# Kernel optimization log

Hardware: AMD Instinct MI355X
Metric: run time of the kernel (lower is better)

The kernel has to match this reference:

```python
import jax, jax.numpy as jnp
import numpy as np
from jax.ops import segment_sum

N0 = 50000
N1 = 50000
E = 300000
D = 128
L = 3
EPS_GIN = 0.1
COEF = 0.1
BN_EPS = 1e-5


def setup_inputs() -> dict:
    key = jax.random.key(0)
    ks = jax.random.split(key, 32)
    inp = {}
    inp['x0'] = jax.random.randint(ks[0], (N0, 2), 0, 3)
    inp['x1'] = jax.random.randint(ks[1], (N1, 2), 0, 3)
    inp['ei101'] = jax.random.randint(ks[2], (2, E), 0, N1)
    inp['ea101'] = jax.random.randint(ks[3], (E, 2), 0, 3)
    inp['ei110'] = jax.random.randint(ks[4], (2, E), 0, N0)  # src '1' -> dst '0' (N1==N0)
    inp['ea110'] = jax.random.randint(ks[5], (E, 2), 0, 3)
    inp['ei021'] = jax.random.randint(ks[6], (2, E), 0, N1)  # src '0' -> dst '1'
    inp['ea021'] = jax.random.randint(ks[7], (E, 2), 0, 3)
    inp['ei030'] = jax.random.randint(ks[8], (2, E), 0, N0)
    inp['ea030'] = jax.random.randint(ks[9], (E, 2), 0, 3)
    # learned parameters
    s = 0.05
    inp['x_emb1'] = jax.random.normal(ks[10], (120, D), jnp.float32) * s
    inp['x_emb2'] = jax.random.normal(ks[11], (3, D), jnp.float32) * s
    inp['e_emb1'] = jax.random.normal(ks[12], (6, D), jnp.float32) * s
    inp['e_emb2'] = jax.random.normal(ks[13], (3, D), jnp.float32) * s
    w = 1.0 / np.sqrt(D)
    inp['gin_w1'] = jax.random.normal(ks[14], (D, 2 * D), jnp.float32) * w
    inp['gin_b1'] = jnp.zeros((2 * D,), jnp.float32)
    inp['gin_w2'] = jax.random.normal(ks[15], (2 * D, D), jnp.float32) * (1.0 / np.sqrt(2 * D))
    inp['gin_b2'] = jnp.zeros((D,), jnp.float32)
    inp['w110'] = jax.random.normal(ks[16], (D, D), jnp.float32) * w
    inp['b110'] = jnp.zeros((D,), jnp.float32)
    inp['w021'] = jax.random.normal(ks[17], (D, D), jnp.float32) * w
    inp['b021'] = jnp.zeros((D,), jnp.float32)
    inp['w030'] = jax.random.normal(ks[18], (D, D), jnp.float32) * w
    inp['b030'] = jnp.zeros((D,), jnp.float32)
    inp['bn_gamma'] = jnp.ones((L, D), jnp.float32)
    inp['bn_beta'] = jnp.zeros((L, D), jnp.float32)
    return inp


def _add_self_loops(ei, ea, n):
    loop = jnp.arange(n, dtype=ei.dtype)
    ei = jnp.concatenate([ei, jnp.stack([loop, loop])], axis=1)
    self_attr = jnp.tile(jnp.array([[4, 0]], dtype=ea.dtype), (n, 1))
    return ei, jnp.concatenate([ea, self_attr], axis=0)


def _bn(x, gamma, beta):
    # training-mode BatchNorm1d: batch statistics, biased variance
    mu = jnp.mean(x, axis=0)
    var = jnp.var(x, axis=0)
    return (x - mu) * jax.lax.rsqrt(var + BN_EPS) * gamma + beta


def reference(x0, x1, ei101, ea101, ei110, ea110, ei021, ea021, ei030, ea030,
              x_emb1, x_emb2, e_emb1, e_emb2,
              gin_w1, gin_b1, gin_w2, gin_b2,
              w110, b110, w021, b021, w030, b030,
              bn_gamma, bn_beta):
    n0, n1 = x0.shape[0], x1.shape[0]
    # AddSelfLoops only for homogeneous edge types, fill_value=[4,0]
    ei101, ea101 = _add_self_loops(ei101, ea101, n1)
    ei030, ea030 = _add_self_loops(ei030, ea030, n0)

    h0 = x_emb1[x0[:, 0]] + x_emb2[x0[:, 1]]
    h1 = x_emb1[x1[:, 0]] + x_emb2[x1[:, 1]]
    e101 = e_emb1[ea101[:, 0]] + e_emb2[ea101[:, 1]]
    e110 = e_emb1[ea110[:, 0]] + e_emb2[ea110[:, 1]]
    e021 = e_emb1[ea021[:, 0]] + e_emb2[ea021[:, 1]]
    e030 = e_emb1[ea030[:, 0]] + e_emb2[ea030[:, 1]]

    def gin(h_src, h_dst, ei, eattr):
        agg = segment_sum(h_src[ei[0]] + eattr, ei[1], num_segments=h_dst.shape[0])
        z = agg + (1.0 + EPS_GIN) * h_dst
        return jnp.maximum(z @ gin_w1 + gin_b1, 0.0) @ gin_w2 + gin_b2

    def lin(h_src, n_dst, ei, eattr, w, b):
        agg = segment_sum(h_src[ei[0]] + eattr, ei[1], num_segments=n_dst)
        return (agg @ w + b) * COEF

    for layer in range(L):
        # HeteroConv aggr='mean' over convs sharing a destination node type
        out1 = 0.5 * (gin(h1, h1, ei101, e101) + lin(h0, n1, ei021, e021, w021, b021))
        out0 = 0.5 * (lin(h1, n0, ei110, e110, w110, b110) + lin(h0, n0, ei030, e030, w030, b030))
        g, b = bn_gamma[layer], bn_beta[layer]
        h0, h1 = _bn(out0, g, b), _bn(out1, g, b)
        if layer < L - 1:
            h0, h1 = jax.nn.relu(h0), jax.nn.relu(h1)
    # to_homogeneous().x: node types in order '0', '1'
    return jnp.concatenate([h0, h1], axis=0)
```

## Files before the change

### kernel.cpp

```cpp
#include <hip/hip_runtime.h>

#define D 128
#define BN_EPS 1e-5f
#define MAXNB 16

typedef __attribute__((ext_vector_type(8))) short bf16x8;
typedef __attribute__((ext_vector_type(4))) float f32x4;

__device__ __forceinline__ unsigned short f2bf(float x) {
  unsigned u = __float_as_uint(x);
  u += 0x7FFF + ((u >> 16) & 1);
  return (unsigned short)(u >> 16);
}
__device__ __forceinline__ float bf2f(unsigned short u) {
  return __uint_as_float((unsigned)u << 16);
}

__global__ __launch_bounds__(256) void k_etbl(const float* __restrict__ e1,
                                              const float* __restrict__ e2,
                                              float* __restrict__ etbl) {
  int idx = blockIdx.x * 256 + threadIdx.x;
  if (idx < 9 * D) {
    int combo = idx / D, c = idx % D;
    etbl[idx] = e1[(combo / 3) * D + c] + e2[(combo % 3) * D + c];
  } else if (idx < 10 * D) {
    int c = idx - 9 * D;
    etbl[idx] = e1[4 * D + c] + e2[c];
  }
}

__global__ __launch_bounds__(256) void k_embed(const int* __restrict__ x,
                                               const float* __restrict__ emb1,
                                               const float* __restrict__ emb2,
                                               unsigned short* __restrict__ out,
                                               int n) {
  int idx = blockIdx.x * 256 + threadIdx.x;
  if (idx >= n * 32) return;
  int node = idx >> 5, c4 = idx & 31;
  int i1 = x[2 * node], i2 = x[2 * node + 1];
  float4 v1 = *(const float4*)(emb1 + (size_t)i1 * D + c4 * 4);
  float4 v2 = *(const float4*)(emb2 + (size_t)i2 * D + c4 * 4);
  ushort4 o;
  o.x = f2bf(v1.x + v2.x); o.y = f2bf(v1.y + v2.y);
  o.z = f2bf(v1.z + v2.z); o.w = f2bf(v1.w + v2.w);
  *(ushort4*)(out + (size_t)node * D + c4 * 4) = o;
}

__global__ __launch_bounds__(256) void k_wprep(const float* __restrict__ W,
                                               unsigned short* __restrict__ Wt,
                                               int K, int N, float scale) {
  int idx = blockIdx.x * 256 + threadIdx.x;
  if (idx >= K * N) return;
  int n = idx / K, k = idx - n * K;
  Wt[idx] = f2bf(W[(size_t)k * N + n] * scale);
}

__global__ __launch_bounds__(256) void k_bprep(
    const float* __restrict__ b110, const float* __restrict__ b030,
    const float* __restrict__ gb1, const float* __restrict__ gb2,
    const float* __restrict__ b021, float* __restrict__ bias0,
    float* __restrict__ biash, float* __restrict__ bias1) {
  int i = threadIdx.x;
  if (i < 128) {
    bias0[i] = 0.05f * (b110[i] + b030[i]);
    bias1[i] = 0.5f * gb2[i] + 0.05f * b021[i];
  }
  biash[i] = gb1[i];
}

struct EdgeArr {
  const int* ei[4];
  const int* ea[4];
  int* cur[4];
  int* pay[4];
};
struct CsrPtrs {
  int* cur[4];
  int* rp[4];
  int n[4];
};

__global__ __launch_bounds__(256) void k_hist4(EdgeArr A, int E) {
  int t = blockIdx.y;
  int e = blockIdx.x * 256 + threadIdx.x;
  if (e >= E) return;
  atomicAdd(&A.cur[t][A.ei[t][E + e]], 1);
}

__global__ __launch_bounds__(256) void k_scan1(CsrPtrs p, int* __restrict__ bsum) {
  __shared__ int lds[256];
  int type = blockIdx.y;
  const int* cur = p.cur[type];
  int n = p.n[type];
  int base = blockIdx.x * 4096;
  int s = 0;
  for (int i = threadIdx.x; i < 4096; i += 256) {
    int idx = base + i;
    if (idx < n) s += cur[idx];
  }
  int tid = threadIdx.x;
  lds[tid] = s;
  __syncthreads();
  for (int off = 128; off > 0; off >>= 1) {
    if (tid < off) lds[tid] += lds[tid + off];
    __syncthreads();
  }
  if (tid == 0) bsum[type * MAXNB + blockIdx.x] = lds[0];
}

__global__ __launch_bounds__(64) void k_scan2(int* __restrict__ bsum) {
  int t = threadIdx.x;
  if (t < 4) {
    int run = 0;
    for (int i = 0; i < MAXNB; ++i) {
      int v = bsum[t * MAXNB + i];
      bsum[t * MAXNB + i] = run;
      run += v;
    }
  }
}

__global__ __launch_bounds__(256) void k_scan3(CsrPtrs p,
                                               const int* __restrict__ bsum,
                                               int E) {
  __shared__ int lds[256];
  int type = blockIdx.y;
  int* cur = p.cur[type];
  int* rp = p.rp[type];
  int n = p.n[type];
  int tid = threadIdx.x;
  if (blockIdx.x == 0 && tid == 0) rp[n] = E;
  int t0 = blockIdx.x * 4096 + tid * 16;
  int loc[16];
  int s = 0;
#pragma unroll
  for (int j = 0; j < 16; ++j) {
    int idx = t0 + j;
    int v = (idx < n) ? cur[idx] : 0;
    loc[j] = s;
    s += v;
  }
  lds[tid] = s;
  __syncthreads();
  for (int off = 1; off < 256; off <<= 1) {
    int v = (tid >= off) ? lds[tid - off] : 0;
    __syncthreads();
    lds[tid] += v;
    __syncthreads();
  }
  int off0 = bsum[type * MAXNB + blockIdx.x] + ((tid == 0) ? 0 : lds[tid - 1]);
#pragma unroll
  for (int j = 0; j < 16; ++j) {
    int idx = t0 + j;
    if (idx < n) {
      int v = off0 + loc[j];
      rp[idx] = v;
      cur[idx] = v;
    }
  }
}

__global__ __launch_bounds__(256) void k_fill4(EdgeArr A, int E) {
  int t = blockIdx.y;
  int e = blockIdx.x * 256 + threadIdx.x;
  if (e >= E) return;
  const int* ei = A.ei[t];
  const int* ea = A.ea[t];
  int dst = ei[E + e];
  int src = ei[e];
  int combo = ea[2 * e] * 3 + ea[2 * e + 1];
  int pos = atomicAdd(&A.cur[t][dst], 1);
  A.pay[t][pos] = src | (combo << 16);
}

struct GArgs {
  const unsigned short* src[4];
  const unsigned short* ini[4];
  const float* bnp[4];
  const int* rp[4];
  const int* pay[4];
  unsigned short* agg[4];
  int mode[4];
  int n[4];
  int norm;
};

__device__ __forceinline__ void cvt8(float (&f)[8], bf16x8 r) {
  const unsigned* u = (const unsigned*)&r;
#pragma unroll
  for (int j = 0; j < 4; ++j) {
    f[2 * j] = __uint_as_float(u[j] << 16);
    f[2 * j + 1] = __uint_as_float(u[j] & 0xFFFF0000u);
  }
}

__device__ __forceinline__ void addrow(float (&acc)[8], bf16x8 r,
                                       const float* etp, const float (&sc)[8],
                                       const float (&sh)[8], bool norm) {
  float f[8];
  cvt8(f, r);
  if (norm) {
#pragma unroll
    for (int j = 0; j < 8; ++j) f[j] = fmaxf(fmaf(f[j], sc[j], sh[j]), 0.f);
  }
  float4 ea = *(const float4*)etp;
  float4 eb = *(const float4*)(etp + 4);
  acc[0] += f[0] + ea.x; acc[1] += f[1] + ea.y;
  acc[2] += f[2] + ea.z; acc[3] += f[3] + ea.w;
  acc[4] += f[4] + eb.x; acc[5] += f[5] + eb.y;
  acc[6] += f[6] + eb.z; acc[7] += f[7] + eb.w;
}

__global__ __launch_bounds__(256) void k_gather_all(GArgs G,
                                                    const float* __restrict__ etbl) {
  __shared__ float et[10 * D];
  for (int i = threadIdx.x; i < 10 * D; i += 256) et[i] = etbl[i];
  __syncthreads();
  int t = blockIdx.y;
  int g = blockIdx.x * 16 + (threadIdx.x >> 4);
  if (g >= G.n[t]) return;
  int l = threadIdx.x & 15;
  int c = l * 8;
  const unsigned short* __restrict__ hsrc = G.src[t];
  const int* __restrict__ pay = G.pay[t];
  bool norm = G.norm != 0;

  float sc[8], sh[8];
  if (norm) {
    const float* bnp = G.bnp[t];
#pragma unroll
    for (int j = 0; j < 8; ++j) { sc[j] = bnp[c + j]; sh[j] = bnp[D + c + j]; }
  } else {
#pragma unroll
    for (int j = 0; j < 8; ++j) { sc[j] = 1.f; sh[j] = 0.f; }
  }

  float acc[8];
  int mode = G.mode[t];
  if (mode == 0) {
#pragma unroll
    for (int j = 0; j < 8; ++j) acc[j] = 0.f;
  } else {
    bf16x8 hv = *(const bf16x8*)(G.ini[t] + (size_t)g * D + c);
    float f[8];
    cvt8(f, hv);
    if (norm) {
#pragma unroll
      for (int j = 0; j < 8; ++j) f[j] = fmaxf(fmaf(f[j], sc[j], sh[j]), 0.f);
    }
    float m = (mode == 2) ? 2.1f : 1.0f;
#pragma unroll
    for (int j = 0; j < 8; ++j) acc[j] = m * f[j] + et[9 * D + c + j];
  }

  int e0 = G.rp[t][g], e1 = G.rp[t][g + 1];
  int e = e0;
  while (e < e1) {
    int cnt = min(16, e1 - e);
    int pv = (e + l < e1) ? pay[e + l] : 0;
    int j = 0;
    for (; j + 3 < cnt; j += 4) {
      int p0 = __shfl(pv, j, 16);
      int p1 = __shfl(pv, j + 1, 16);
      int p2 = __shfl(pv, j + 2, 16);
      int p3 = __shfl(pv, j + 3, 16);
      bf16x8 r0 = *(const bf16x8*)(hsrc + (size_t)(p0 & 0xFFFF) * D + c);
      bf16x8 r1 = *(const bf16x8*)(hsrc + (size_t)(p1 & 0xFFFF) * D + c);
      bf16x8 r2 = *(const bf16x8*)(hsrc + (size_t)(p2 & 0xFFFF) * D + c);
      bf16x8 r3 = *(const bf16x8*)(hsrc + (size_t)(p3 & 0xFFFF) * D + c);
      addrow(acc, r0, et + (p0 >> 16) * D + c, sc, sh, norm);
      addrow(acc, r1, et + (p1 >> 16) * D + c, sc, sh, norm);
      addrow(acc, r2, et + (p2 >> 16) * D + c, sc, sh, norm);
      addrow(acc, r3, et + (p3 >> 16) * D + c, sc, sh, norm);
    }
    for (; j < cnt; ++j) {
      int p0 = __shfl(pv, j, 16);
      bf16x8 r0 = *(const bf16x8*)(hsrc + (size_t)(p0 & 0xFFFF) * D + c);
      addrow(acc, r0, et + (p0 >> 16) * D + c, sc, sh, norm);
    }
    e += cnt;
  }

  unsigned o0 = (unsigned)f2bf(acc[0]) | ((unsigned)f2bf(acc[1]) << 16);
  unsigned o1 = (unsigned)f2bf(acc[2]) | ((unsigned)f2bf(acc[3]) << 16);
  unsigned o2 = (unsigned)f2bf(acc[4]) | ((unsigned)f2bf(acc[5]) << 16);
  unsigned o3 = (unsigned)f2bf(acc[6]) | ((unsigned)f2bf(acc[7]) << 16);
  *(uint4*)(G.agg[t] + (size_t)g * D + c) = make_uint4(o0, o1, o2, o3);
}

template <int NCOLS, int K1, int K2, bool RELU, bool STATS, bool OBF16>
__global__ __launch_bounds__(256) void gemm_breg(
    const unsigned short* __restrict__ A1, const unsigned short* __restrict__ Wt1,
    const unsigned short* __restrict__ A2, const unsigned short* __restrict__ Wt2,
    const float* __restrict__ bias, void* __restrict__ Cv, int M,
    float* __restrict__ stats) {
  constexpr int WC = NCOLS / 4;
  constexpr int CF = WC / 16;
  constexpr int KF1 = K1 / 32;
  constexpr int KF2 = (K2 > 0) ? (K2 / 32) : 1;

  int tid = threadIdx.x;
  int w = tid >> 6, l = tid & 63;
  int lr = l & 15, lk = l >> 4;
  int colbase = w * WC;
  int row0 = blockIdx.x * 64;

  f32x4 acc[4][CF];
#pragma unroll
  for (int rf = 0; rf < 4; ++rf)
#pragma unroll
    for (int cf = 0; cf < CF; ++cf) acc[rf][cf] = (f32x4)(0.f);

  {
    const unsigned short* ap[4];
#pragma unroll
    for (int rf = 0; rf < 4; ++rf) {
      int r = row0 + rf * 16 + lr;
      if (r > M - 1) r = M - 1;
      ap[rf] = A1 + (size_t)r * K1 + lk * 8;
    }
    bf16x8 B[CF][KF1];
#pragma unroll
    for (int cf = 0; cf < CF; ++cf)
#pragma unroll
      for (int kf = 0; kf < KF1; ++kf)
        B[cf][kf] = *(const bf16x8*)(Wt1 + (size_t)(colbase + cf * 16 + lr) * K1 +
                                     kf * 32 + lk * 8);
#pragma unroll
    for (int kf = 0; kf < KF1; ++kf) {
      bf16x8 a[4];
#pragma unroll
      for (int rf = 0; rf < 4; ++rf) a[rf] = *(const bf16x8*)(ap[rf] + kf * 32);
#pragma unroll
      for (int rf = 0; rf < 4; ++rf)
#pragma unroll
        for (int cf = 0; cf < CF; ++cf)
          acc[rf][cf] = __builtin_amdgcn_mfma_f32_16x16x32_bf16(a[rf], B[cf][kf],
                                                                acc[rf][cf], 0, 0, 0);
    }
  }
  if constexpr (K2 > 0) {
    const unsigned short* ap[4];
#pragma unroll
    for (int rf = 0; rf < 4; ++rf) {
      int r = row0 + rf * 16 + lr;
      if (r > M - 1) r = M - 1;
      ap[rf] = A2 + (size_t)r * K2 + lk * 8;
    }
    bf16x8 B[CF][KF2];
#pragma unroll
    for (int cf = 0; cf < CF; ++cf)
#pragma unroll
      for (int kf = 0; kf < KF2; ++kf)
        B[cf][kf] = *(const bf16x8*)(Wt2 + (size_t)(colbase + cf * 16 + lr) * K2 +
                                     kf * 32 + lk * 8);
#pragma unroll
    for (int kf = 0; kf < KF2; ++kf) {
      bf16x8 a[4];
#pragma unroll
      for (int rf = 0; rf < 4; ++rf) a[rf] = *(const bf16x8*)(ap[rf] + kf * 32);
#pragma unroll
      for (int rf = 0; rf < 4; ++rf)
#pragma unroll
        for (int cf = 0; cf < CF; ++cf)
          acc[rf][cf] = __builtin_amdgcn_mfma_f32_16x16x32_bf16(a[rf], B[cf][kf],
                                                                acc[rf][cf], 0, 0, 0);
    }
  }

  float bv[CF];
#pragma unroll
  for (int cf = 0; cf < CF; ++cf) bv[cf] = bias[colbase + cf * 16 + lr];

  float colS[CF], colQ[CF];
#pragma unroll
  for (int cf = 0; cf < CF; ++cf) { colS[cf] = 0.f; colQ[cf] = 0.f; }

  float* Cf = (float*)Cv;
  unsigned short* Cb = (unsigned short*)Cv;
#pragma unroll
  for (int rf = 0; rf < 4; ++rf) {
#pragma unroll
    for (int r = 0; r < 4; ++r) {
      int row = row0 + rf * 16 + lk * 4 + r;
      bool ok = row < M;
#pragma unroll
      for (int cf = 0; cf < CF; ++cf) {
        int col = colbase + cf * 16 + lr;
        float v = acc[rf][cf][r] + bv[cf];
        if (RELU) v = fmaxf(v, 0.f);
        if (ok) {
          if (OBF16)
            Cb[(size_t)row * NCOLS + col] = f2bf(v);
          else
            Cf[(size_t)row * NCOLS + col] = v;
          if (STATS) { colS[cf] += v; colQ[cf] += v * v; }
        }
      }
    }
  }

  if constexpr (STATS) {
#pragma unroll
    for (int cf = 0; cf < CF; ++cf) {
      float s = colS[cf], q = colQ[cf];
      s += __shfl_xor(s, 16); q += __shfl_xor(q, 16);
      s += __shfl_xor(s, 32); q += __shfl_xor(q, 32);
      if (lk == 0) {
        int col = colbase + cf * 16 + lr;
        atomicAdd(&stats[col], s);
        atomicAdd(&stats[D + col], q);
      }
    }
  }
}

__global__ __launch_bounds__(256) void k_bnprep(const float* __restrict__ stats,
                                                const float* __restrict__ gamma,
                                                const float* __restrict__ beta,
                                                float* __restrict__ bnp0,
                                                float* __restrict__ bnp1,
                                                float invM0, float invM1) {
  int i = threadIdx.x;
  if (i < 128) {
    float mu = stats[i] * invM0;
    float var = stats[D + i] * invM0 - mu * mu;
    float sc = rsqrtf(var + BN_EPS) * gamma[i];
    bnp0[i] = sc;
    bnp0[D + i] = beta[i] - mu * sc;
  } else {
    int d = i - 128;
    float mu = stats[2 * D + d] * invM1;
    float var = stats[3 * D + d] * invM1 - mu * mu;
    float sc = rsqrtf(var + BN_EPS) * gamma[d];
    bnp1[d] = sc;
    bnp1[D + d] = beta[d] - mu * sc;
  }
}

__global__ __launch_bounds__(256) void k_bnfin(float* __restrict__ X, int M,
                                               const float* __restrict__ bnp) {
  int idx = blockIdx.x * 256 + threadIdx.x;
  int i = idx >> 5, c4 = idx & 31;
  if (i >= M) return;
  float4 v = *(float4*)(X + (size_t)i * D + c4 * 4);
  float4 sc = *(const float4*)(bnp + c4 * 4);
  float4 sh = *(const float4*)(bnp + D + c4 * 4);
  float4 o;
  o.x = fmaf(v.x, sc.x, sh.x); o.y = fmaf(v.y, sc.y, sh.y);
  o.z = fmaf(v.z, sc.z, sh.z); o.w = fmaf(v.w, sc.w, sh.w);
  *(float4*)(X + (size_t)i * D + c4 * 4) = o;
}

extern "C" void kernel_launch(void* const* d_in, const int* in_sizes, int n_in,
                              void* d_out, int out_size, void* d_ws,
                              size_t ws_size, hipStream_t stream) {
  const int* x0 = (const int*)d_in[0];
  const int* x1 = (const int*)d_in[1];
  const int* ei101 = (const int*)d_in[2];
  const int* ea101 = (const int*)d_in[3];
  const int* ei110 = (const int*)d_in[4];
  const int* ea110 = (const int*)d_in[5];
  const int* ei021 = (const int*)d_in[6];
  const int* ea021 = (const int*)d_in[7];
  const int* ei030 = (const int*)d_in[8];
  const int* ea030 = (const int*)d_in[9];
  const float* x_emb1 = (const float*)d_in[10];
  const float* x_emb2 = (const float*)d_in[11];
  const float* e_emb1 = (const float*)d_in[12];
  const float* e_emb2 = (const float*)d_in[13];
  const float* gin_w1 = (const float*)d_in[14];
  const float* gin_b1 = (const float*)d_in[15];
  const float* gin_w2 = (const float*)d_in[16];
  const float* gin_b2 = (const float*)d_in[17];
  const float* w110 = (const float*)d_in[18];
  const float* b110 = (const float*)d_in[19];
  const float* w021 = (const float*)d_in[20];
  const float* b021 = (const float*)d_in[21];
  const float* w030 = (const float*)d_in[22];
  const float* b030 = (const float*)d_in[23];
  const float* bn_gamma = (const float*)d_in[24];
  const float* bn_beta = (const float*)d_in[25];

  int n0 = in_sizes[0] / 2, n1 = in_sizes[1] / 2;
  int E = in_sizes[2] / 2;
  int nmax = n0 > n1 ? n0 : n1;

  float* h0f = (float*)d_out;
  float* h1f = h0f + (size_t)n0 * D;

  char* p = (char*)d_ws;
  auto alloc = [&](size_t bytes) {
    char* r = p;
    p += (bytes + 63) & ~(size_t)63;
    return r;
  };
  unsigned short* h0r = (unsigned short*)alloc((size_t)n0 * D * 2);
  unsigned short* h1r = (unsigned short*)alloc((size_t)n1 * D * 2);
  unsigned short* z1b = (unsigned short*)alloc((size_t)n1 * D * 2);
  unsigned short* a021b = (unsigned short*)alloc((size_t)n1 * D * 2);
  unsigned short* a110b = (unsigned short*)alloc((size_t)n0 * D * 2);
  unsigned short* a030b = (unsigned short*)alloc((size_t)n0 * D * 2);
  unsigned short* hiddenb = (unsigned short*)alloc((size_t)n1 * 256 * 2);
  float* etbl = (float*)alloc(10 * D * 4);
  float* stats = (float*)alloc(4 * D * 4);
  float* bnp0 = (float*)alloc(2 * D * 4);
  float* bnp1 = (float*)alloc(2 * D * 4);
  unsigned short* wt110 = (unsigned short*)alloc(128 * 128 * 2);
  unsigned short* wt030 = (unsigned short*)alloc(128 * 128 * 2);
  unsigned short* wt021 = (unsigned short*)alloc(128 * 128 * 2);
  unsigned short* wtg1 = (unsigned short*)alloc(256 * 128 * 2);
  unsigned short* wtg2 = (unsigned short*)alloc(128 * 256 * 2);
  float* bias0 = (float*)alloc(128 * 4);
  float* biash = (float*)alloc(256 * 4);
  float* bias1 = (float*)alloc(128 * 4);

  EdgeArr EA;
  CsrPtrs cp;
  const int* eis[4] = {ei101, ei021, ei110, ei030};
  const int* eas[4] = {ea101, ea021, ea110, ea030};
  int ndst[4] = {n1, n1, n0, n0};
  for (int t = 0; t < 4; ++t) {
    cp.rp[t] = (int*)alloc((size_t)(nmax + 1) * 4);
    cp.cur[t] = (int*)alloc((size_t)nmax * 4);
    EA.pay[t] = (int*)alloc((size_t)E * 4);
    cp.n[t] = ndst[t];
    EA.ei[t] = eis[t];
    EA.ea[t] = eas[t];
    EA.cur[t] = cp.cur[t];
  }
  int* bsum = (int*)alloc(4 * MAXNB * 4);

  dim3 b256(256);
  int eBlocks = (E + 255) / 256;

  k_etbl<<<5, b256, 0, stream>>>(e_emb1, e_emb2, etbl);
  k_embed<<<(n0 * 32 + 255) / 256, b256, 0, stream>>>(x0, x_emb1, x_emb2, h0r, n0);
  k_embed<<<(n1 * 32 + 255) / 256, b256, 0, stream>>>(x1, x_emb1, x_emb2, h1r, n1);
  k_wprep<<<64, b256, 0, stream>>>(w110, wt110, 128, 128, 0.05f);
  k_wprep<<<64, b256, 0, stream>>>(w030, wt030, 128, 128, 0.05f);
  k_wprep<<<64, b256, 0, stream>>>(w021, wt021, 128, 128, 0.05f);
  k_wprep<<<128, b256, 0, stream>>>(gin_w1, wtg1, 128, 256, 1.0f);
  k_wprep<<<128, b256, 0, stream>>>(gin_w2, wtg2, 256, 128, 0.5f);
  k_bprep<<<1, b256, 0, stream>>>(b110, b030, gin_b1, gin_b2, b021, bias0, biash, bias1);

  for (int t = 0; t < 4; ++t)
    hipMemsetAsync(cp.cur[t], 0, (size_t)ndst[t] * sizeof(int), stream);
  k_hist4<<<dim3(eBlocks, 4), b256, 0, stream>>>(EA, E);
  hipMemsetAsync(bsum, 0, 4 * MAXNB * sizeof(int), stream);
  int nb = (nmax + 4095) / 4096;
  k_scan1<<<dim3(nb, 4), b256, 0, stream>>>(cp, bsum);
  k_scan2<<<1, dim3(64), 0, stream>>>(bsum);
  k_scan3<<<dim3(nb, 4), b256, 0, stream>>>(cp, bsum, E);
  k_fill4<<<dim3(eBlocks, 4), b256, 0, stream>>>(EA, E);

  GArgs GA;
  GA.src[0] = h1r; GA.ini[0] = h1r;     GA.bnp[0] = bnp1; GA.agg[0] = z1b;   GA.mode[0] = 2; GA.n[0] = n1;
  GA.src[1] = h0r; GA.ini[1] = nullptr; GA.bnp[1] = bnp0; GA.agg[1] = a021b; GA.mode[1] = 0; GA.n[1] = n1;
  GA.src[2] = h1r; GA.ini[2] = nullptr; GA.bnp[2] = bnp1; GA.agg[2] = a110b; GA.mode[2] = 0; GA.n[2] = n0;
  GA.src[3] = h0r; GA.ini[3] = h0r;     GA.bnp[3] = bnp0; GA.agg[3] = a030b; GA.mode[3] = 1; GA.n[3] = n0;
  for (int t = 0; t < 4; ++t) {
    GA.rp[t] = cp.rp[t];
    GA.pay[t] = EA.pay[t];
  }

  int mB0 = (n0 + 63) / 64, mB1 = (n1 + 63) / 64;
  dim3 gGrid((nmax + 15) / 16, 4);

  for (int layer = 0; layer < 3; ++layer) {
    GA.norm = (layer > 0) ? 1 : 0;
    k_gather_all<<<gGrid, b256, 0, stream>>>(GA, etbl);

    hipMemsetAsync(stats, 0, 4 * D * sizeof(float), stream);

    if (layer < 2) {
      gemm_breg<128, 128, 128, false, true, true><<<mB0, b256, 0, stream>>>(
          a110b, wt110, a030b, wt030, bias0, h0r, n0, stats);
      gemm_breg<256, 128, 0, true, false, true><<<mB1, b256, 0, stream>>>(
          z1b, wtg1, nullptr, nullptr, biash, hiddenb, n1, nullptr);
      gemm_breg<128, 256, 128, false, true, true><<<mB1, b256, 0, stream>>>(
          hiddenb, wtg2, a021b, wt021, bias1, h1r, n1, stats + 2 * D);
    } else {
      gemm_breg<128, 128, 128, false, true, false><<<mB0, b256, 0, stream>>>(
          a110b, wt110, a030b, wt030, bias0, h0f, n0, stats);
      gemm_breg<256, 128, 0, true, false, true><<<mB1, b256, 0, stream>>>(
          z1b, wtg1, nullptr, nullptr, biash, hiddenb, n1, nullptr);
      gemm_breg<128, 256, 128, false, true, false><<<mB1, b256, 0, stream>>>(
          hiddenb, wtg2, a021b, wt021, bias1, h1f, n1, stats + 2 * D);
    }

    k_bnprep<<<1, b256, 0, stream>>>(stats, bn_gamma + layer * D,
                                     bn_beta + layer * D, bnp0, bnp1,
                                     1.0f / n0, 1.0f / n1);
    if (layer == 2) {
      k_bnfin<<<(n0 * 32 + 255) / 256, b256, 0, stream>>>(h0f, n0, bnp0);
      k_bnfin<<<(n1 * 32 + 255) / 256, b256, 0, stream>>>(h1f, n1, bnp1);
    }
  }
}
```

Measured before the change: 780.2 us.

## Prenormalize node features once and split each node's edges across four lane groups

The BatchNorm+ReLU that was applied to every gathered neighbour row inside the gather kernel is moved into a separate k_hnorm pass, which writes normalized bf16 copies of the features once per layer. The gather kernel is restructured so that each wave handles four consecutive nodes. For each node, four 16-lane groups take interleaved edges and are reduced with xor shuffles, raising memory-level parallelism for low-degree nodes. In exchange, this adds an extra elementwise pass, extra workspace buffers, and cross-lane reductions. The same grid size is kept, so each block now covers 16 nodes via 4 waves × 4 nodes.

```diff
diff --git a/kernel.cpp b/kernel.cpp
--- a/kernel.cpp
+++ b/kernel.cpp
@@ -12,8 +12,14 @@
   u += 0x7FFF + ((u >> 16) & 1);
   return (unsigned short)(u >> 16);
 }
-__device__ __forceinline__ float bf2f(unsigned short u) {
-  return __uint_as_float((unsigned)u << 16);
+
+__device__ __forceinline__ void cvt8(float (&f)[8], bf16x8 r) {
+  const unsigned* u = (const unsigned*)&r;
+#pragma unroll
+  for (int j = 0; j < 4; ++j) {
+    f[2 * j] = __uint_as_float(u[j] << 16);
+    f[2 * j + 1] = __uint_as_float(u[j] & 0xFFFF0000u);
+  }
 }
 
 __global__ __launch_bounds__(256) void k_etbl(const float* __restrict__ e1,
@@ -173,36 +179,39 @@
   A.pay[t][pos] = src | (combo << 16);
 }
 
+__global__ __launch_bounds__(256) void k_hnorm(const unsigned short* __restrict__ h,
+                                               unsigned short* __restrict__ hn,
+                                               const float* __restrict__ bnp,
+                                               int n) {
+  int idx = blockIdx.x * 256 + threadIdx.x;
+  if (idx >= n * 16) return;
+  int node = idx >> 4, sl = idx & 15, c = sl * 8;
+  bf16x8 v = *(const bf16x8*)(h + (size_t)node * D + c);
+  float f[8];
+  cvt8(f, v);
+  unsigned o[4];
+#pragma unroll
+  for (int j = 0; j < 4; ++j) {
+    float a = fmaxf(fmaf(f[2 * j], bnp[c + 2 * j], bnp[D + c + 2 * j]), 0.f);
+    float b = fmaxf(fmaf(f[2 * j + 1], bnp[c + 2 * j + 1], bnp[D + c + 2 * j + 1]), 0.f);
+    o[j] = (unsigned)f2bf(a) | ((unsigned)f2bf(b) << 16);
+  }
+  *(uint4*)(hn + (size_t)node * D + c) = make_uint4(o[0], o[1], o[2], o[3]);
+}
+
 struct GArgs {
   const unsigned short* src[4];
-  const unsigned short* ini[4];
-  const float* bnp[4];
   const int* rp[4];
   const int* pay[4];
   unsigned short* agg[4];
   int mode[4];
   int n[4];
-  int norm;
 };
 
-__device__ __forceinline__ void cvt8(float (&f)[8], bf16x8 r) {
-  const unsigned* u = (const unsigned*)&r;
-#pragma unroll
-  for (int j = 0; j < 4; ++j) {
-    f[2 * j] = __uint_as_float(u[j] << 16);
-    f[2 * j + 1] = __uint_as_float(u[j] & 0xFFFF0000u);
-  }
-}
-
-__device__ __forceinline__ void addrow(float (&acc)[8], bf16x8 r,
-                                       const float* etp, const float (&sc)[8],
-                                       const float (&sh)[8], bool norm) {
+__device__ __forceinline__ void addet(float (&acc)[8], bf16x8 r,
+                                      const float* etp) {
   float f[8];
   cvt8(f, r);
-  if (norm) {
-#pragma unroll
-    for (int j = 0; j < 8; ++j) f[j] = fmaxf(fmaf(f[j], sc[j], sh[j]), 0.f);
-  }
   float4 ea = *(const float4*)etp;
   float4 eb = *(const float4*)(etp + 4);
   acc[0] += f[0] + ea.x; acc[1] += f[1] + ea.y;
@@ -217,75 +226,61 @@
   for (int i = threadIdx.x; i < 10 * D; i += 256) et[i] = etbl[i];
   __syncthreads();
   int t = blockIdx.y;
-  int g = blockIdx.x * 16 + (threadIdx.x >> 4);
-  if (g >= G.n[t]) return;
-  int l = threadIdx.x & 15;
-  int c = l * 8;
+  int n = G.n[t];
+  int wv = threadIdx.x >> 6;
+  int l = threadIdx.x & 63;
+  int grp = l >> 4, sl = l & 15, c = sl * 8;
   const unsigned short* __restrict__ hsrc = G.src[t];
   const int* __restrict__ pay = G.pay[t];
-  bool norm = G.norm != 0;
-
-  float sc[8], sh[8];
-  if (norm) {
-    const float* bnp = G.bnp[t];
-#pragma unroll
-    for (int j = 0; j < 8; ++j) { sc[j] = bnp[c + j]; sh[j] = bnp[D + c + j]; }
-  } else {
-#pragma unroll
-    for (int j = 0; j < 8; ++j) { sc[j] = 1.f; sh[j] = 0.f; }
-  }
-
-  float acc[8];
+  const int* __restrict__ rp = G.rp[t];
+  unsigned short* __restrict__ agg = G.agg[t];
   int mode = G.mode[t];
-  if (mode == 0) {
-#pragma unroll
-    for (int j = 0; j < 8; ++j) acc[j] = 0.f;
-  } else {
-    bf16x8 hv = *(const bf16x8*)(G.ini[t] + (size_t)g * D + c);
-    float f[8];
-    cvt8(f, hv);
-    if (norm) {
-#pragma unroll
-      for (int j = 0; j < 8; ++j) f[j] = fmaxf(fmaf(f[j], sc[j], sh[j]), 0.f);
-    }
-    float m = (mode == 2) ? 2.1f : 1.0f;
-#pragma unroll
-    for (int j = 0; j < 8; ++j) acc[j] = m * f[j] + et[9 * D + c + j];
-  }
-
-  int e0 = G.rp[t][g], e1 = G.rp[t][g + 1];
-  int e = e0;
-  while (e < e1) {
-    int cnt = min(16, e1 - e);
-    int pv = (e + l < e1) ? pay[e + l] : 0;
-    int j = 0;
-    for (; j + 3 < cnt; j += 4) {
-      int p0 = __shfl(pv, j, 16);
-      int p1 = __shfl(pv, j + 1, 16);
-      int p2 = __shfl(pv, j + 2, 16);
-      int p3 = __shfl(pv, j + 3, 16);
+  int gbase = (blockIdx.x * 4 + wv) * 4;
+
+  for (int i = 0; i < 4; ++i) {
+    int g = gbase + i;
+    if (g >= n) break;
+    float acc[8];
+    if (grp == 0 && mode != 0) {
+      bf16x8 hv = *(const bf16x8*)(hsrc + (size_t)g * D + c);
+      float f[8];
+      cvt8(f, hv);
+      float m = (mode == 2) ? 2.1f : 1.0f;
+#pragma unroll
+      for (int j = 0; j < 8; ++j) acc[j] = m * f[j] + et[9 * D + c + j];
+    } else {
+#pragma unroll
+      for (int j = 0; j < 8; ++j) acc[j] = 0.f;
+    }
+    int e1 = rp[g + 1];
+    int e = rp[g] + grp;
+    while (e + 4 < e1) {
+      int p0 = pay[e];
+      int p1 = pay[e + 4];
       bf16x8 r0 = *(const bf16x8*)(hsrc + (size_t)(p0 & 0xFFFF) * D + c);
       bf16x8 r1 = *(const bf16x8*)(hsrc + (size_t)(p1 & 0xFFFF) * D + c);
-      bf16x8 r2 = *(const bf16x8*)(hsrc + (size_t)(p2 & 0xFFFF) * D + c);
-      bf16x8 r3 = *(const bf16x8*)(hsrc + (size_t)(p3 & 0xFFFF) * D + c);
-      addrow(acc, r0, et + (p0 >> 16) * D + c, sc, sh, norm);
-      addrow(acc, r1, et + (p1 >> 16) * D + c, sc, sh, norm);
-      addrow(acc, r2, et + (p2 >> 16) * D + c, sc, sh, norm);
-      addrow(acc, r3, et + (p3 >> 16) * D + c, sc, sh, norm);
-    }
-    for (; j < cnt; ++j) {
-      int p0 = __shfl(pv, j, 16);
+      addet(acc, r0, et + (p0 >> 16) * D + c);
+      addet(acc, r1, et + (p1 >> 16) * D + c);
+      e += 8;
+    }
+    if (e < e1) {
+      int p0 = pay[e];
       bf16x8 r0 = *(const bf16x8*)(hsrc + (size_t)(p0 & 0xFFFF) * D + c);
-      addrow(acc, r0, et + (p0 >> 16) * D + c, sc, sh, norm);
-    }
-    e += cnt;
-  }
-
-  unsigned o0 = (unsigned)f2bf(acc[0]) | ((unsigned)f2bf(acc[1]) << 16);
-  unsigned o1 = (unsigned)f2bf(acc[2]) | ((unsigned)f2bf(acc[3]) << 16);
-  unsigned o2 = (unsigned)f2bf(acc[4]) | ((unsigned)f2bf(acc[5]) << 16);
-  unsigned o3 = (unsigned)f2bf(acc[6]) | ((unsigned)f2bf(acc[7]) << 16);
-  *(uint4*)(G.agg[t] + (size_t)g * D + c) = make_uint4(o0, o1, o2, o3);
+      addet(acc, r0, et + (p0 >> 16) * D + c);
+    }
+#pragma unroll
+    for (int j = 0; j < 8; ++j) {
+      acc[j] += __shfl_xor(acc[j], 16);
+      acc[j] += __shfl_xor(acc[j], 32);
+    }
+    if (grp == 0) {
+      unsigned o0 = (unsigned)f2bf(acc[0]) | ((unsigned)f2bf(acc[1]) << 16);
+      unsigned o1 = (unsigned)f2bf(acc[2]) | ((unsigned)f2bf(acc[3]) << 16);
+      unsigned o2 = (unsigned)f2bf(acc[4]) | ((unsigned)f2bf(acc[5]) << 16);
+      unsigned o3 = (unsigned)f2bf(acc[6]) | ((unsigned)f2bf(acc[7]) << 16);
+      *(uint4*)(agg + (size_t)g * D + c) = make_uint4(o0, o1, o2, o3);
+    }
+  }
 }
 
 template <int NCOLS, int K1, int K2, bool RELU, bool STATS, bool OBF16>
@@ -497,6 +492,8 @@
   };
   unsigned short* h0r = (unsigned short*)alloc((size_t)n0 * D * 2);
   unsigned short* h1r = (unsigned short*)alloc((size_t)n1 * D * 2);
+  unsigned short* hn0 = (unsigned short*)alloc((size_t)n0 * D * 2);
+  unsigned short* hn1 = (unsigned short*)alloc((size_t)n1 * D * 2);
   unsigned short* z1b = (unsigned short*)alloc((size_t)n1 * D * 2);
   unsigned short* a021b = (unsigned short*)alloc((size_t)n1 * D * 2);
   unsigned short* a110b = (unsigned short*)alloc((size_t)n0 * D * 2);
@@ -555,10 +552,10 @@
   k_fill4<<<dim3(eBlocks, 4), b256, 0, stream>>>(EA, E);
 
   GArgs GA;
-  GA.src[0] = h1r; GA.ini[0] = h1r;     GA.bnp[0] = bnp1; GA.agg[0] = z1b;   GA.mode[0] = 2; GA.n[0] = n1;
-  GA.src[1] = h0r; GA.ini[1] = nullptr; GA.bnp[1] = bnp0; GA.agg[1] = a021b; GA.mode[1] = 0; GA.n[1] = n1;
-  GA.src[2] = h1r; GA.ini[2] = nullptr; GA.bnp[2] = bnp1; GA.agg[2] = a110b; GA.mode[2] = 0; GA.n[2] = n0;
-  GA.src[3] = h0r; GA.ini[3] = h0r;     GA.bnp[3] = bnp0; GA.agg[3] = a030b; GA.mode[3] = 1; GA.n[3] = n0;
+  GA.agg[0] = z1b;   GA.mode[0] = 2; GA.n[0] = n1;
+  GA.agg[1] = a021b; GA.mode[1] = 0; GA.n[1] = n1;
+  GA.agg[2] = a110b; GA.mode[2] = 0; GA.n[2] = n0;
+  GA.agg[3] = a030b; GA.mode[3] = 1; GA.n[3] = n0;
   for (int t = 0; t < 4; ++t) {
     GA.rp[t] = cp.rp[t];
     GA.pay[t] = EA.pay[t];
@@ -568,7 +565,9 @@
   dim3 gGrid((nmax + 15) / 16, 4);
 
   for (int layer = 0; layer < 3; ++layer) {
-    GA.norm = (layer > 0) ? 1 : 0;
+    const unsigned short* s0 = (layer == 0) ? h0r : hn0;
+    const unsigned short* s1 = (layer == 0) ? h1r : hn1;
+    GA.src[0] = s1; GA.src[1] = s0; GA.src[2] = s1; GA.src[3] = s0;
     k_gather_all<<<gGrid, b256, 0, stream>>>(GA, etbl);
 
     hipMemsetAsync(stats, 0, 4 * D * sizeof(float), stream);
@@ -592,7 +591,10 @@
     k_bnprep<<<1, b256, 0, stream>>>(stats, bn_gamma + layer * D,
                                      bn_beta + layer * D, bnp0, bnp1,
                                      1.0f / n0, 1.0f / n1);
-    if (layer == 2) {
+    if (layer < 2) {
+      k_hnorm<<<(n0 * 16 + 255) / 256, b256, 0, stream>>>(h0r, hn0, bnp0, n0);
+      k_hnorm<<<(n1 * 16 + 255) / 256, b256, 0, stream>>>(h1r, hn1, bnp1, n1);
+    } else {
       k_bnfin<<<(n0 * 32 + 255) / 256, b256, 0, stream>>>(h0f, n0, bnp0);
       k_bnfin<<<(n1 * 32 + 255) / 256, b256, 0, stream>>>(h1f, n1, bnp1);
     }
```

Result: slower. 799.2 us (+2.4%).
